# Kernel tuning notes

Hardware: AMD Instinct MI355X
Metric: run time of the kernel (lower is better)

Reference implementation:

```python
import jax, jax.numpy as jnp
import numpy as np

B, S, D, H = 2, 2048, 2048, 16
HD = D // H


def setup_inputs() -> dict:
    key = jax.random.key(0)
    ks = jax.random.split(key, 9)
    scale = 0.02
    return {
        "x": jax.random.normal(ks[0], (B, S, D), dtype=jnp.float32),
        "wq_w": jax.random.normal(ks[1], (D, D), dtype=jnp.float32) * scale,
        "wq_b": jnp.zeros((D,), dtype=jnp.float32),
        "wk_w": jax.random.normal(ks[2], (D, D), dtype=jnp.float32) * scale,
        "wk_b": jnp.zeros((D,), dtype=jnp.float32),
        "wv_w": jax.random.normal(ks[3], (D, D), dtype=jnp.float32) * scale,
        "wv_b": jnp.zeros((D,), dtype=jnp.float32),
        "wo_w": jax.random.normal(ks[4], (D, D), dtype=jnp.float32) * scale,
        "wo_b": jnp.zeros((D,), dtype=jnp.float32),
    }


def reference(x, wq_w, wq_b, wk_w, wk_b, wv_w, wv_b, wo_w, wo_b):
    # torch Linear: y = x @ W.T + b
    q = x @ wq_w.T + wq_b  # [B,S,D]
    k = x @ wk_w.T + wk_b
    v = x @ wv_w.T + wv_b
    # [B,S,D] -> [B,H,S,HD]
    q = q.reshape(B, S, H, HD).transpose(0, 2, 1, 3)
    k = k.reshape(B, S, H, HD).transpose(0, 2, 1, 3)
    v = v.reshape(B, S, H, HD).transpose(0, 2, 1, 3)
    # scores [B,H,S,S], scaled by sqrt(d_dim) as in the original (not head_dim)
    scores = jnp.einsum("bhid,bhjd->bhij", q, k) / np.float32(np.sqrt(D))
    # faithful reproduction of the module's triu/transpose masking:
    m = jnp.swapaxes(jnp.triu(scores), -2, -1)  # lower-tri, zeros elsewhere
    p = jax.nn.softmax(m, axis=-2)              # softmax over dim=-2, zeros included
    a = jnp.swapaxes(jnp.triu(p), -2, -1)       # [B,H,S,S]
    attn = jnp.einsum("bhij,bhjd->bhid", a, v)  # [B,H,S,HD]
    concat = attn.transpose(0, 2, 1, 3).reshape(B, S, D)
    return concat @ wo_w.T + wo_b
```

## Files before the change

### kernel.cpp

```cpp
#include <hip/hip_runtime.h>

#define BB 2
#define SS 2048
#define DD 2048
#define HH 16
#define HDIM 128
#define MTOK (BB*SS)
#define BHH (BB*HH)
#define NCHUNK 16
#define QKN (2*DD)

typedef __attribute__((ext_vector_type(8))) __bf16 bf16x8;
typedef __attribute__((ext_vector_type(4))) float f32x4;
typedef __attribute__((ext_vector_type(8))) int i32x8;
typedef __attribute__((ext_vector_type(4))) int i32x4;

__device__ __forceinline__ unsigned short f2bf(float f) {
  unsigned u = __float_as_uint(f);
  u += 0x7FFFu + ((u >> 16) & 1u);
  return (unsigned short)(u >> 16);
}
__device__ __forceinline__ float bf2f(unsigned short s) {
  return __uint_as_float(((unsigned)s) << 16);
}
__device__ __forceinline__ unsigned char f2e4m3(float f) {
  int pk = __builtin_amdgcn_cvt_pk_fp8_f32(f, f, 0, false);
  return (unsigned char)(pk & 0xFF);
}

#define GLOAD_LDS16(src, dst)                                                   \
  __builtin_amdgcn_global_load_lds(                                             \
      (const void __attribute__((address_space(1)))*)(src),                     \
      (void __attribute__((address_space(3)))*)(dst), 16, 0, 0)

__device__ __forceinline__ void barrier_raw() {
  asm volatile("" ::: "memory");
  __builtin_amdgcn_s_barrier();
  asm volatile("" ::: "memory");
}

__global__ void cvt_x_dual(const float* __restrict__ in,
                           unsigned short* __restrict__ outb,
                           unsigned int* __restrict__ out8, int n4) {
  int i = blockIdx.x * blockDim.x + threadIdx.x;
  if (i < n4) {
    float4 v = ((const float4*)in)[i];
    ushort4 o;
    o.x = f2bf(v.x); o.y = f2bf(v.y); o.z = f2bf(v.z); o.w = f2bf(v.w);
    ((ushort4*)outb)[i] = o;
    int p0 = __builtin_amdgcn_cvt_pk_fp8_f32(v.x, v.y, 0, false);
    int p1 = __builtin_amdgcn_cvt_pk_fp8_f32(v.z, v.w, 0, false);
    out8[i] = (unsigned)(p0 & 0xFFFF) | ((unsigned)(p1 & 0xFFFF) << 16);
  }
}

__global__ void cvt_wqk8(const float* __restrict__ a, const float* __restrict__ b,
                         unsigned int* __restrict__ out) {
  int i = blockIdx.x * blockDim.x + threadIdx.x;
  int sel = i >> 20, r = i & 0xFFFFF;
  const float* src = sel == 0 ? a : b;
  float4 v = ((const float4*)src)[r];
  int p0 = __builtin_amdgcn_cvt_pk_fp8_f32(v.x, v.y, 0, false);
  int p1 = __builtin_amdgcn_cvt_pk_fp8_f32(v.z, v.w, 0, false);
  out[i] = (unsigned)(p0 & 0xFFFF) | ((unsigned)(p1 & 0xFFFF) << 16);
}

__global__ void cvt_w2bf(const float* __restrict__ a, const float* __restrict__ b,
                         unsigned short* __restrict__ out) {
  int i = blockIdx.x * blockDim.x + threadIdx.x;
  int sel = i >> 20, r = i & 0xFFFFF;
  const float* src = sel == 0 ? a : b;
  float4 v = ((const float4*)src)[r];
  ushort4 o;
  o.x = f2bf(v.x); o.y = f2bf(v.y); o.z = f2bf(v.z); o.w = f2bf(v.w);
  ((ushort4*)out)[i] = o;
}

__global__ void concat2(const float* __restrict__ a, const float* __restrict__ b,
                        float* __restrict__ out) {
  int i = blockIdx.x * blockDim.x + threadIdx.x;
  if (i < DD) { out[i] = a[i]; out[DD + i] = b[i]; }
}

template <bool OUT_BF16>
__global__ __launch_bounds__(512, 1) void gemm_bt8(
    const __bf16* __restrict__ A, const __bf16* __restrict__ W,
    const float* __restrict__ bias, void* __restrict__ Cout,
    int M, int N, int K) {
  __shared__ unsigned char lds[2][49152];
  const int t = threadIdx.x;
  const int lane = t & 63, wave = t >> 6;
  const int quad = lane >> 4, l16 = lane & 15;
  const int bid = blockIdx.x;
  const int swz = (bid & 7) * 32 + (bid >> 3);
  const int m0 = (swz >> 4) * 256;
  const int n0 = (swz & 15) * 128;
  const int wm = (wave >> 1) * 64;
  const int wn = (wave & 1) * 64;

  const __bf16* sA[4];
#pragma unroll
  for (int c = 0; c < 4; ++c) {
    int L = c * 512 + t;
    int row = L >> 3, p = L & 7;
    sA[c] = A + (size_t)(m0 + row) * K + ((p ^ (row & 7)) * 8);
  }
  const __bf16* sB[2];
#pragma unroll
  for (int c = 0; c < 2; ++c) {
    int L = c * 512 + t;
    int row = L >> 3, p = L & 7;
    sB[c] = W + (size_t)(n0 + row) * K + ((p ^ (row & 7)) * 8);
  }
  const int phk0 = (quad ^ (l16 & 7)) * 16;
  const int phk1 = ((4 + quad) ^ (l16 & 7)) * 16;

  f32x4 acc[4][4] = {};

  const int NT = K >> 6;

#pragma unroll
  for (int c = 0; c < 4; ++c)
    GLOAD_LDS16(sA[c], &lds[0][c * 8192 + wave * 1024]);
#pragma unroll
  for (int c = 0; c < 2; ++c)
    GLOAD_LDS16(sB[c], &lds[0][32768 + c * 8192 + wave * 1024]);

  for (int tt = 0; tt < NT; ++tt) {
    const int cur = tt & 1;
    const bool pf = (tt + 1 < NT);
    const int k1 = (tt + 1) << 6;

    if (pf) {
#pragma unroll
      for (int c = 0; c < 4; ++c)
        GLOAD_LDS16(sA[c] + k1, &lds[cur ^ 1][c * 8192 + wave * 1024]);
      asm volatile("s_waitcnt vmcnt(4)" ::: "memory");
    } else {
      asm volatile("s_waitcnt vmcnt(0)" ::: "memory");
    }
    barrier_raw();
    {
      bf16x8 af[4], bfv[4];
#pragma unroll
      for (int mt = 0; mt < 4; ++mt)
        af[mt] = *(const bf16x8*)&lds[cur][(wm + mt * 16 + l16) * 128 + phk0];
#pragma unroll
      for (int nt = 0; nt < 4; ++nt)
        bfv[nt] = *(const bf16x8*)&lds[cur][32768 + (wn + nt * 16 + l16) * 128 + phk0];
      __builtin_amdgcn_s_setprio(1);
#pragma unroll
      for (int mt = 0; mt < 4; ++mt)
#pragma unroll
        for (int nt = 0; nt < 4; ++nt)
          acc[mt][nt] = __builtin_amdgcn_mfma_f32_16x16x32_bf16(
              af[mt], bfv[nt], acc[mt][nt], 0, 0, 0);
      __builtin_amdgcn_s_setprio(0);
    }

    if (pf) {
#pragma unroll
      for (int c = 0; c < 2; ++c)
        GLOAD_LDS16(sB[c] + k1, &lds[cur ^ 1][32768 + c * 8192 + wave * 1024]);
    }
    barrier_raw();
    {
      bf16x8 af[4], bfv[4];
#pragma unroll
      for (int mt = 0; mt < 4; ++mt)
        af[mt] = *(const bf16x8*)&lds[cur][(wm + mt * 16 + l16) * 128 + phk1];
#pragma unroll
      for (int nt = 0; nt < 4; ++nt)
        bfv[nt] = *(const bf16x8*)&lds[cur][32768 + (wn + nt * 16 + l16) * 128 + phk1];
      __builtin_amdgcn_s_setprio(1);
#pragma unroll
      for (int mt = 0; mt < 4; ++mt)
#pragma unroll
        for (int nt = 0; nt < 4; ++nt)
          acc[mt][nt] = __builtin_amdgcn_mfma_f32_16x16x32_bf16(
              af[mt], bfv[nt], acc[mt][nt], 0, 0, 0);
      __builtin_amdgcn_s_setprio(0);
    }
    barrier_raw();
  }

#pragma unroll
  for (int mt = 0; mt < 4; ++mt) {
#pragma unroll
    for (int nt = 0; nt < 4; ++nt) {
      int col = n0 + wn + nt * 16 + l16;
      float bv = bias[col];
#pragma unroll
      for (int r = 0; r < 4; ++r) {
        int row = m0 + wm + mt * 16 + quad * 4 + r;
        float v = acc[mt][nt][r] + bv;
        if constexpr (OUT_BF16)
          ((unsigned short*)Cout)[(size_t)row * N + col] = f2bf(v);
        else
          ((float*)Cout)[(size_t)row * N + col] = v;
      }
    }
  }
}

__global__ __launch_bounds__(512, 1) void gemm_qk8(
    const unsigned char* __restrict__ A8, const unsigned char* __restrict__ W8,
    const float* __restrict__ bias, unsigned char* __restrict__ Cout,
    int M, int N, int K) {
  __shared__ unsigned char lds[2][49152];
  const int t = threadIdx.x;
  const int lane = t & 63, wave = t >> 6;
  const int quad = lane >> 4, l16 = lane & 15;
  const int m0 = blockIdx.y * 256;
  const int n0 = blockIdx.x * 128;
  const int wm = (wave >> 1) * 64;
  const int wn = (wave & 1) * 64;

  const unsigned char* sA[4];
#pragma unroll
  for (int c = 0; c < 4; ++c) {
    int L = c * 512 + t;
    int row = L >> 3, p = L & 7;
    sA[c] = A8 + (size_t)(m0 + row) * K + ((p ^ (row & 7)) * 16);
  }
  const unsigned char* sB[2];
#pragma unroll
  for (int c = 0; c < 2; ++c) {
    int L = c * 512 + t;
    int row = L >> 3, p = L & 7;
    sB[c] = W8 + (size_t)(n0 + row) * K + ((p ^ (row & 7)) * 16);
  }
  const int p0 = (2 * quad) ^ (l16 & 7);

  f32x4 acc[4][4] = {};

  const int NT = K >> 7;

#pragma unroll
  for (int c = 0; c < 4; ++c)
    GLOAD_LDS16(sA[c], &lds[0][c * 8192 + wave * 1024]);
#pragma unroll
  for (int c = 0; c < 2; ++c)
    GLOAD_LDS16(sB[c], &lds[0][32768 + c * 8192 + wave * 1024]);

  for (int tt = 0; tt < NT; ++tt) {
    const int cur = tt & 1;
    const bool pf = (tt + 1 < NT);
    const int k1 = (tt + 1) << 7;

    if (pf) {
#pragma unroll
      for (int c = 0; c < 4; ++c)
        GLOAD_LDS16(sA[c] + k1, &lds[cur ^ 1][c * 8192 + wave * 1024]);
      asm volatile("s_waitcnt vmcnt(4)" ::: "memory");
    } else {
      asm volatile("s_waitcnt vmcnt(0)" ::: "memory");
    }
    barrier_raw();
    i32x8 af[4];
    {
#pragma unroll
      for (int mt = 0; mt < 4; ++mt) {
        int ra = (wm + mt * 16 + l16) * 128 + p0 * 16;
        ((i32x4*)&af[mt])[0] = *(const i32x4*)&lds[cur][ra];
        ((i32x4*)&af[mt])[1] = *(const i32x4*)&lds[cur][ra ^ 16];
      }
      i32x8 bv[2];
#pragma unroll
      for (int nt = 0; nt < 2; ++nt) {
        int rb = 32768 + (wn + nt * 16 + l16) * 128 + p0 * 16;
        ((i32x4*)&bv[nt])[0] = *(const i32x4*)&lds[cur][rb];
        ((i32x4*)&bv[nt])[1] = *(const i32x4*)&lds[cur][rb ^ 16];
      }
      __builtin_amdgcn_s_setprio(1);
#pragma unroll
      for (int mt = 0; mt < 4; ++mt)
#pragma unroll
        for (int nt = 0; nt < 2; ++nt)
          acc[mt][nt] = __builtin_amdgcn_mfma_scale_f32_16x16x128_f8f6f4(
              af[mt], bv[nt], acc[mt][nt], 0, 0, 0, 127, 0, 127);
      __builtin_amdgcn_s_setprio(0);
    }

    if (pf) {
#pragma unroll
      for (int c = 0; c < 2; ++c)
        GLOAD_LDS16(sB[c] + k1, &lds[cur ^ 1][32768 + c * 8192 + wave * 1024]);
    }
    barrier_raw();
    {
      i32x8 bv[2];
#pragma unroll
      for (int nt = 0; nt < 2; ++nt) {
        int rb = 32768 + (wn + (nt + 2) * 16 + l16) * 128 + p0 * 16;
        ((i32x4*)&bv[nt])[0] = *(const i32x4*)&lds[cur][rb];
        ((i32x4*)&bv[nt])[1] = *(const i32x4*)&lds[cur][rb ^ 16];
      }
      __builtin_amdgcn_s_setprio(1);
#pragma unroll
      for (int mt = 0; mt < 4; ++mt)
#pragma unroll
        for (int nt = 0; nt < 2; ++nt)
          acc[mt][nt + 2] = __builtin_amdgcn_mfma_scale_f32_16x16x128_f8f6f4(
              af[mt], bv[nt], acc[mt][nt + 2], 0, 0, 0, 127, 0, 127);
      __builtin_amdgcn_s_setprio(0);
    }
    barrier_raw();
  }

#pragma unroll
  for (int mt = 0; mt < 4; ++mt) {
#pragma unroll
    for (int nt = 0; nt < 4; ++nt) {
      int col = n0 + wn + nt * 16 + l16;
      float bv = bias[col];
#pragma unroll
      for (int r = 0; r < 4; ++r) {
        int row = m0 + wm + mt * 16 + quad * 4 + r;
        Cout[(size_t)row * N + col] = f2e4m3(acc[mt][nt][r] + bv);
      }
    }
  }
}

__global__ __launch_bounds__(256, 4) void qk_rowsum8(
    const unsigned char* __restrict__ q8, const unsigned char* __restrict__ k8,
    float* __restrict__ denomA, float* __restrict__ denomB,
    float* __restrict__ diag) {
  __shared__ unsigned char lK[2][128 * 128];
  __shared__ float redS[4][64];
  __shared__ float redD[4][64];
  const int t = threadIdx.x;
  const int lane = t & 63, wave = t >> 6;
  const int quad = lane >> 4, l16 = lane & 15;
  const int bh = blockIdx.y;
  const int b = bh >> 4, h = bh & 15;
  const int pair = blockIdx.x >> 1;
  const int half = blockIdx.x & 1;
  const float C = 0.03187935771f;
  const f32x4 fz = {0.f, 0.f, 0.f, 0.f};

  int soff[4];
#pragma unroll
  for (int c = 0; c < 4; ++c) {
    int L = c * 256 + t;
    int row = L >> 3, p = L & 7;
    soff[c] = row * QKN + ((p ^ (row & 7)) * 16);
  }
  const int p0 = (2 * quad) ^ (l16 & 7);
  int bo[2];
#pragma unroll
  for (int nt = 0; nt < 2; ++nt)
    bo[nt] = (wave * 32 + nt * 16 + l16) * 128 + p0 * 16;

  const unsigned char* kbase = k8 + (size_t)(b * SS) * QKN + h * HDIM;

  for (int sub = 0; sub < 2; ++sub) {
    const int tile = (sub == 0) ? pair : 31 - pair;
    const int i0 = tile * 64;
    const int jbase = i0 & ~127;
    const int ntile = (SS - jbase) >> 7;

    i32x8 af[4];
    {
      const unsigned char* qbase =
          q8 + (size_t)(b * SS + i0 + l16) * QKN + h * HDIM + quad * 32;
#pragma unroll
      for (int mt = 0; mt < 4; ++mt)
        af[mt] = *(const i32x8*)(qbase + (size_t)(mt * 16) * QKN);
    }

    float rowacc[4][4] = {};

    int kidx = half;
    if (kidx < ntile) {
      {
        const unsigned char* src = kbase + (size_t)(jbase + kidx * 128) * QKN;
#pragma unroll
        for (int c = 0; c < 4; ++c)
          GLOAD_LDS16(src + soff[c], &lK[0][(c * 256 + wave * 64) * 16]);
      }
      asm volatile("s_waitcnt vmcnt(0)" ::: "memory");
      __syncthreads();
      int cur = 0;
      for (; kidx < ntile; kidx += 2, cur ^= 1) {
        if (kidx + 2 < ntile) {
          const unsigned char* src =
              kbase + (size_t)(jbase + (kidx + 2) * 128) * QKN;
#pragma unroll
          for (int c = 0; c < 4; ++c)
            GLOAD_LDS16(src + soff[c], &lK[cur ^ 1][(c * 256 + wave * 64) * 16]);
        }
        const unsigned char* lkc = lK[cur];
        const int j0 = jbase + kidx * 128;
        if (kidx == 0) {
          float dloc[4][4] = {};
#pragma unroll
          for (int nt = 0; nt < 2; ++nt) {
            i32x8 bf;
            ((i32x4*)&bf)[0] = *(const i32x4*)(lkc + bo[nt]);
            ((i32x4*)&bf)[1] = *(const i32x4*)(lkc + (bo[nt] ^ 16));
            f32x4 acc[4];
#pragma unroll
            for (int mt = 0; mt < 4; ++mt)
              acc[mt] = __builtin_amdgcn_mfma_scale_f32_16x16x128_f8f6f4(
                  af[mt], bf, fz, 0, 0, 0, 127, 0, 127);
            const int colg = j0 + wave * 32 + nt * 16 + l16;
#pragma unroll
            for (int mt = 0; mt < 4; ++mt)
#pragma unroll
              for (int r = 0; r < 4; ++r) {
                int rg = i0 + mt * 16 + quad * 4 + r;
                float e = (colg >= rg)
                              ? __builtin_amdgcn_exp2f(acc[mt][r] * C) : 0.f;
                rowacc[mt][r] += e;
                if (colg == rg) dloc[mt][r] = e;
              }
          }
#pragma unroll
          for (int mt = 0; mt < 4; ++mt)
#pragma unroll
            for (int r = 0; r < 4; ++r) {
              float d = dloc[mt][r];
#pragma unroll
              for (int off = 1; off < 16; off <<= 1) d += __shfl_xor(d, off, 64);
              if (l16 == 0) redD[wave][mt * 16 + quad * 4 + r] = d;
            }
        } else {
#pragma unroll
          for (int nt = 0; nt < 2; ++nt) {
            i32x8 bf;
            ((i32x4*)&bf)[0] = *(const i32x4*)(lkc + bo[nt]);
            ((i32x4*)&bf)[1] = *(const i32x4*)(lkc + (bo[nt] ^ 16));
            f32x4 acc[4];
#pragma unroll
            for (int mt = 0; mt < 4; ++mt)
              acc[mt] = __builtin_amdgcn_mfma_scale_f32_16x16x128_f8f6f4(
                  af[mt], bf, fz, 0, 0, 0, 127, 0, 127);
#pragma unroll
            for (int mt = 0; mt < 4; ++mt)
#pragma unroll
              for (int r = 0; r < 4; ++r)
                rowacc[mt][r] += __builtin_amdgcn_exp2f(acc[mt][r] * C);
          }
        }
        asm volatile("s_waitcnt vmcnt(0)" ::: "memory");
        __syncthreads();
      }
    }

    __syncthreads();
#pragma unroll
    for (int mt = 0; mt < 4; ++mt)
#pragma unroll
      for (int r = 0; r < 4; ++r) {
        float s = rowacc[mt][r];
#pragma unroll
        for (int off = 1; off < 16; off <<= 1) s += __shfl_xor(s, off, 64);
        if (l16 == 0) redS[wave][mt * 16 + quad * 4 + r] = s;
      }
    __syncthreads();
    if (t < 64) {
      const int rg = i0 + t;
      float s = redS[0][t] + redS[1][t] + redS[2][t] + redS[3][t];
      if (half == 0) {
        denomA[bh * SS + rg] = (float)rg + s;
        diag[bh * SS + rg] = redD[0][t] + redD[1][t] + redD[2][t] + redD[3][t];
      } else {
        denomB[bh * SS + rg] = s;
      }
    }
  }
}

__global__ void scan_pass1(const __bf16* __restrict__ v0,
                           float* __restrict__ csum) {
  int blk = blockIdx.x;
  int bh = blk >> 4, c = blk & 15;
  int b = bh >> 4, h = bh & 15;
  int t = threadIdx.x;
  int rs = t >> 4, dg = t & 15;
  const unsigned short* base = (const unsigned short*)v0 +
      (size_t)(b * SS + c * 128 + rs * 8) * DD + h * HDIM + dg * 8;
  float s[8] = {0.f, 0.f, 0.f, 0.f, 0.f, 0.f, 0.f, 0.f};
#pragma unroll
  for (int i = 0; i < 8; ++i) {
    uint4 u = *(const uint4*)(base + (size_t)i * DD);
    const unsigned short* us = (const unsigned short*)&u;
#pragma unroll
    for (int j = 0; j < 8; ++j) s[j] += bf2f(us[j]);
  }
  __shared__ float red[16 * 128];
#pragma unroll
  for (int j = 0; j < 8; ++j) red[rs * 128 + dg * 8 + j] = s[j];
  __syncthreads();
  for (int st = 8; st >= 1; st >>= 1) {
    if (rs < st) {
#pragma unroll
      for (int j = 0; j < 8; ++j)
        red[rs * 128 + dg * 8 + j] += red[(rs + st) * 128 + dg * 8 + j];
    }
    __syncthreads();
  }
  if (rs == 0) {
#pragma unroll
    for (int j = 0; j < 8; ++j)
      csum[(size_t)blk * 128 + dg * 8 + j] = red[dg * 8 + j];
  }
}

__global__ void scan_pass2(const __bf16* __restrict__ v0,
                           const float* __restrict__ csum,
                           const float* __restrict__ denomA,
                           const float* __restrict__ denomB,
                           const float* __restrict__ diag,
                           unsigned short* __restrict__ ctx) {
  int blk = blockIdx.x;
  int bh = blk >> 4, c = blk & 15;
  int b = bh >> 4, h = bh & 15;
  int t = threadIdx.x;
  int rs = t >> 4, dg = t & 15;
  const unsigned short* vbase = (const unsigned short*)v0 +
      (size_t)(b * SS + c * 128 + rs * 8) * DD + h * HDIM + dg * 8;
  float vrow[8][8];
  float ls[8] = {0.f, 0.f, 0.f, 0.f, 0.f, 0.f, 0.f, 0.f};
#pragma unroll
  for (int i = 0; i < 8; ++i) {
    uint4 u = *(const uint4*)(vbase + (size_t)i * DD);
    const unsigned short* us = (const unsigned short*)&u;
#pragma unroll
    for (int j = 0; j < 8; ++j) {
      vrow[i][j] = bf2f(us[j]);
      ls[j] += vrow[i][j];
    }
  }
  __shared__ float red[16 * 128];
#pragma unroll
  for (int j = 0; j < 8; ++j) red[rs * 128 + dg * 8 + j] = ls[j];
  __syncthreads();

  float pre[8] = {0.f, 0.f, 0.f, 0.f, 0.f, 0.f, 0.f, 0.f};
  for (int cc = 0; cc < c; ++cc) {
    const float* cp = csum + (size_t)(bh * 16 + cc) * 128 + dg * 8;
#pragma unroll
    for (int j = 0; j < 8; ++j) pre[j] += cp[j];
  }
  for (int ss2 = 0; ss2 < rs; ++ss2) {
#pragma unroll
    for (int j = 0; j < 8; ++j) pre[j] += red[ss2 * 128 + dg * 8 + j];
  }

  int row0 = c * 128 + rs * 8;
  unsigned short* obase =
      ctx + (size_t)(b * SS + row0) * DD + h * HDIM + dg * 8;
  const float* dnA = denomA + bh * SS + row0;
  const float* dnB = denomB + bh * SS + row0;
  const float* dgp = diag + bh * SS + row0;
#pragma unroll
  for (int i = 0; i < 8; ++i) {
    float inv = 1.0f / (dnA[i] + dnB[i]);
    float dv = dgp[i];
    unsigned short o[8];
#pragma unroll
    for (int j = 0; j < 8; ++j) {
      float val = (pre[j] + dv * vrow[i][j]) * inv;
      o[j] = f2bf(val);
      pre[j] += vrow[i][j];
    }
    *(uint4*)(obase + (size_t)i * DD) = *(const uint4*)o;
  }
}

extern "C" void kernel_launch(void* const* d_in, const int* in_sizes, int n_in,
                              void* d_out, int out_size, void* d_ws, size_t ws_size,
                              hipStream_t stream) {
  (void)in_sizes; (void)n_in; (void)out_size; (void)ws_size;
  const float* x    = (const float*)d_in[0];
  const float* wq_w = (const float*)d_in[1];
  const float* wq_b = (const float*)d_in[2];
  const float* wk_w = (const float*)d_in[3];
  const float* wk_b = (const float*)d_in[4];
  const float* wv_w = (const float*)d_in[5];
  const float* wv_b = (const float*)d_in[6];
  const float* wo_w = (const float*)d_in[7];
  const float* wo_b = (const float*)d_in[8];

  char* ws = (char*)d_ws;
  size_t off = 0;
  auto alloc = [&](size_t bytes) {
    char* p = ws + off;
    off += (bytes + 255) & ~(size_t)255;
    return p;
  };
  unsigned short* xb   = (unsigned short*)alloc((size_t)MTOK * DD * 2);
  unsigned char*  x8   = (unsigned char*)alloc((size_t)MTOK * DD);
  unsigned char*  wqk8 = (unsigned char*)alloc((size_t)2 * DD * DD);
  unsigned short* wvo  = (unsigned short*)alloc((size_t)2 * DD * DD * 2);
  unsigned char*  qk8  = (unsigned char*)alloc((size_t)MTOK * QKN);
  unsigned short* v    = (unsigned short*)alloc((size_t)MTOK * DD * 2);
  unsigned short* ctx  = (unsigned short*)alloc((size_t)MTOK * DD * 2);
  float* biasqk = (float*)alloc((size_t)2 * DD * 4);
  float* denomA = (float*)alloc((size_t)BHH * SS * 4);
  float* denomB = (float*)alloc((size_t)BHH * SS * 4);
  float* diag   = (float*)alloc((size_t)BHH * SS * 4);
  float* csum   = (float*)alloc((size_t)BHH * NCHUNK * 128 * 4);

  {
    int n4 = MTOK * DD / 4;
    cvt_x_dual<<<n4 / 256, 256, 0, stream>>>(x, xb, (unsigned int*)x8, n4);
    cvt_wqk8<<<(2 << 20) / 256, 256, 0, stream>>>(wq_w, wk_w, (unsigned int*)wqk8);
    cvt_w2bf<<<(2 << 20) / 256, 256, 0, stream>>>(wv_w, wo_w, wvo);
    concat2<<<(DD + 255) / 256, 256, 0, stream>>>(wq_b, wk_b, biasqk);
  }

  gemm_qk8<<<dim3(QKN / 128, MTOK / 256), 512, 0, stream>>>(
      x8, wqk8, biasqk, qk8, MTOK, QKN, DD);

  gemm_bt8<true><<<(MTOK / 256) * (DD / 128), 512, 0, stream>>>(
      (const __bf16*)xb, (const __bf16*)wvo, wv_b, v, MTOK, DD, DD);

  qk_rowsum8<<<dim3(32, BHH), 256, 0, stream>>>(
      qk8,
      qk8 + DD,
      denomA, denomB, diag);

  scan_pass1<<<BHH * NCHUNK, 256, 0, stream>>>((const __bf16*)v, csum);
  scan_pass2<<<BHH * NCHUNK, 256, 0, stream>>>((const __bf16*)v, csum,
                                               denomA, denomB, diag, ctx);

  gemm_bt8<false><<<(MTOK / 256) * (DD / 128), 512, 0, stream>>>(
      (const __bf16*)ctx, (const __bf16*)(wvo + (size_t)DD * DD), wo_b,
      d_out, MTOK, DD, DD);
}
```

Measured before the change: 320.0 us.

## Retile FP8 QK GEMM to 128x128 tiles and fuse weight conversion kernels

The FP8 Q/K projection GEMM moves from 256x128 tiles with 512 threads and one block per CU to 128x128 tiles with 256 threads and two blocks per CU. LDS per block shrinks, and the A and B tiles now load symmetrically. This doubles the grid to give better CU balance and lets two blocks overlap, at the cost of less operand reuse per tile. Separately, the three weight and bias conversion kernels are merged into one launch to cut launch overhead.

```diff
diff --git a/kernel.cpp b/kernel.cpp
--- a/kernel.cpp
+++ b/kernel.cpp
@@ -54,32 +54,34 @@
   }
 }
 
-__global__ void cvt_wqk8(const float* __restrict__ a, const float* __restrict__ b,
-                         unsigned int* __restrict__ out) {
-  int i = blockIdx.x * blockDim.x + threadIdx.x;
-  int sel = i >> 20, r = i & 0xFFFFF;
-  const float* src = sel == 0 ? a : b;
-  float4 v = ((const float4*)src)[r];
-  int p0 = __builtin_amdgcn_cvt_pk_fp8_f32(v.x, v.y, 0, false);
-  int p1 = __builtin_amdgcn_cvt_pk_fp8_f32(v.z, v.w, 0, false);
-  out[i] = (unsigned)(p0 & 0xFFFF) | ((unsigned)(p1 & 0xFFFF) << 16);
-}
-
-__global__ void cvt_w2bf(const float* __restrict__ a, const float* __restrict__ b,
-                         unsigned short* __restrict__ out) {
-  int i = blockIdx.x * blockDim.x + threadIdx.x;
-  int sel = i >> 20, r = i & 0xFFFFF;
-  const float* src = sel == 0 ? a : b;
-  float4 v = ((const float4*)src)[r];
-  ushort4 o;
-  o.x = f2bf(v.x); o.y = f2bf(v.y); o.z = f2bf(v.z); o.w = f2bf(v.w);
-  ((ushort4*)out)[i] = o;
-}
-
-__global__ void concat2(const float* __restrict__ a, const float* __restrict__ b,
-                        float* __restrict__ out) {
-  int i = blockIdx.x * blockDim.x + threadIdx.x;
-  if (i < DD) { out[i] = a[i]; out[DD + i] = b[i]; }
+__global__ void cvt_w_all(const float* __restrict__ wq, const float* __restrict__ wk,
+                          const float* __restrict__ wv, const float* __restrict__ wo,
+                          const float* __restrict__ wqb, const float* __restrict__ wkb,
+                          unsigned int* __restrict__ out8,
+                          unsigned short* __restrict__ outb,
+                          float* __restrict__ biasqk) {
+  int blk = blockIdx.x;
+  int tid = threadIdx.x;
+  if (blk < 8192) {
+    int i = blk * 256 + tid;
+    int sel = i >> 20, r = i & 0xFFFFF;
+    const float* src = sel == 0 ? wq : wk;
+    float4 v = ((const float4*)src)[r];
+    int p0 = __builtin_amdgcn_cvt_pk_fp8_f32(v.x, v.y, 0, false);
+    int p1 = __builtin_amdgcn_cvt_pk_fp8_f32(v.z, v.w, 0, false);
+    out8[i] = (unsigned)(p0 & 0xFFFF) | ((unsigned)(p1 & 0xFFFF) << 16);
+  } else if (blk < 16384) {
+    int i = (blk - 8192) * 256 + tid;
+    int sel = i >> 20, r = i & 0xFFFFF;
+    const float* src = sel == 0 ? wv : wo;
+    float4 v = ((const float4*)src)[r];
+    ushort4 o;
+    o.x = f2bf(v.x); o.y = f2bf(v.y); o.z = f2bf(v.z); o.w = f2bf(v.w);
+    ((ushort4*)outb)[i] = o;
+  } else {
+    int i = (blk - 16384) * 256 + tid;
+    biasqk[i] = (i < DD) ? wqb[i] : wkb[i - DD];
+  }
 }
 
 template <bool OUT_BF16>
@@ -203,32 +205,27 @@
   }
 }
 
-__global__ __launch_bounds__(512, 1) void gemm_qk8(
+__global__ __launch_bounds__(256, 2) void gemm_qk8(
     const unsigned char* __restrict__ A8, const unsigned char* __restrict__ W8,
     const float* __restrict__ bias, unsigned char* __restrict__ Cout,
     int M, int N, int K) {
-  __shared__ unsigned char lds[2][49152];
+  __shared__ unsigned char lds[2][32768];
   const int t = threadIdx.x;
   const int lane = t & 63, wave = t >> 6;
   const int quad = lane >> 4, l16 = lane & 15;
-  const int m0 = blockIdx.y * 256;
+  const int m0 = blockIdx.y * 128;
   const int n0 = blockIdx.x * 128;
-  const int wm = (wave >> 1) * 64;
-  const int wn = (wave & 1) * 64;
+  const int wm = (wave & 1) * 64, wn = (wave >> 1) * 64;
 
   const unsigned char* sA[4];
+  const unsigned char* sB[4];
 #pragma unroll
   for (int c = 0; c < 4; ++c) {
-    int L = c * 512 + t;
+    int L = c * 256 + t;
     int row = L >> 3, p = L & 7;
-    sA[c] = A8 + (size_t)(m0 + row) * K + ((p ^ (row & 7)) * 16);
-  }
-  const unsigned char* sB[2];
-#pragma unroll
-  for (int c = 0; c < 2; ++c) {
-    int L = c * 512 + t;
-    int row = L >> 3, p = L & 7;
-    sB[c] = W8 + (size_t)(n0 + row) * K + ((p ^ (row & 7)) * 16);
+    int sc = (p ^ (row & 7)) * 16;
+    sA[c] = A8 + (size_t)(m0 + row) * K + sc;
+    sB[c] = W8 + (size_t)(n0 + row) * K + sc;
   }
   const int p0 = (2 * quad) ^ (l16 & 7);
 
@@ -238,10 +235,10 @@
 
 #pragma unroll
   for (int c = 0; c < 4; ++c)
-    GLOAD_LDS16(sA[c], &lds[0][c * 8192 + wave * 1024]);
-#pragma unroll
-  for (int c = 0; c < 2; ++c)
-    GLOAD_LDS16(sB[c], &lds[0][32768 + c * 8192 + wave * 1024]);
+    GLOAD_LDS16(sA[c], &lds[0][(c * 256 + wave * 64) * 16]);
+#pragma unroll
+  for (int c = 0; c < 4; ++c)
+    GLOAD_LDS16(sB[c], &lds[0][16384 + (c * 256 + wave * 64) * 16]);
 
   for (int tt = 0; tt < NT; ++tt) {
     const int cur = tt & 1;
@@ -251,7 +248,7 @@
     if (pf) {
 #pragma unroll
       for (int c = 0; c < 4; ++c)
-        GLOAD_LDS16(sA[c] + k1, &lds[cur ^ 1][c * 8192 + wave * 1024]);
+        GLOAD_LDS16(sA[c] + k1, &lds[cur ^ 1][(c * 256 + wave * 64) * 16]);
       asm volatile("s_waitcnt vmcnt(4)" ::: "memory");
     } else {
       asm volatile("s_waitcnt vmcnt(0)" ::: "memory");
@@ -268,7 +265,7 @@
       i32x8 bv[2];
 #pragma unroll
       for (int nt = 0; nt < 2; ++nt) {
-        int rb = 32768 + (wn + nt * 16 + l16) * 128 + p0 * 16;
+        int rb = 16384 + (wn + nt * 16 + l16) * 128 + p0 * 16;
         ((i32x4*)&bv[nt])[0] = *(const i32x4*)&lds[cur][rb];
         ((i32x4*)&bv[nt])[1] = *(const i32x4*)&lds[cur][rb ^ 16];
       }
@@ -284,15 +281,15 @@
 
     if (pf) {
 #pragma unroll
-      for (int c = 0; c < 2; ++c)
-        GLOAD_LDS16(sB[c] + k1, &lds[cur ^ 1][32768 + c * 8192 + wave * 1024]);
+      for (int c = 0; c < 4; ++c)
+        GLOAD_LDS16(sB[c] + k1, &lds[cur ^ 1][16384 + (c * 256 + wave * 64) * 16]);
     }
     barrier_raw();
     {
       i32x8 bv[2];
 #pragma unroll
       for (int nt = 0; nt < 2; ++nt) {
-        int rb = 32768 + (wn + (nt + 2) * 16 + l16) * 128 + p0 * 16;
+        int rb = 16384 + (wn + (nt + 2) * 16 + l16) * 128 + p0 * 16;
         ((i32x4*)&bv[nt])[0] = *(const i32x4*)&lds[cur][rb];
         ((i32x4*)&bv[nt])[1] = *(const i32x4*)&lds[cur][rb ^ 16];
       }
@@ -608,12 +605,11 @@
   {
     int n4 = MTOK * DD / 4;
     cvt_x_dual<<<n4 / 256, 256, 0, stream>>>(x, xb, (unsigned int*)x8, n4);
-    cvt_wqk8<<<(2 << 20) / 256, 256, 0, stream>>>(wq_w, wk_w, (unsigned int*)wqk8);
-    cvt_w2bf<<<(2 << 20) / 256, 256, 0, stream>>>(wv_w, wo_w, wvo);
-    concat2<<<(DD + 255) / 256, 256, 0, stream>>>(wq_b, wk_b, biasqk);
-  }
-
-  gemm_qk8<<<dim3(QKN / 128, MTOK / 256), 512, 0, stream>>>(
+    cvt_w_all<<<16400, 256, 0, stream>>>(wq_w, wk_w, wv_w, wo_w, wq_b, wk_b,
+                                         (unsigned int*)wqk8, wvo, biasqk);
+  }
+
+  gemm_qk8<<<dim3(QKN / 128, MTOK / 128), 256, 0, stream>>>(
       x8, wqk8, biasqk, qk8, MTOK, QKN, DD);
 
   gemm_bt8<true><<<(MTOK / 256) * (DD / 128), 512, 0, stream>>>(
```

Result: no change. 316.3 us (-1.2%).
